# Performance work log

Measured on AMD Instinct MI355X. Metric: run time of the kernel, lower is better.

## Reference

```python
import jax, jax.numpy as jnp
import numpy as np

N, E, D, H, C, G = 20000, 160000, 128, 4, 3, 512
IN_F, EF = 74, 11


def setup_inputs():
    key = jax.random.key(0)
    ks = jax.random.split(key, 20)
    rn = lambda k, shape, s=0.05: jax.random.normal(k, shape, jnp.float32) * s
    return {
        "h0": rn(ks[0], (N, IN_F), 1.0),
        "e_f": rn(ks[1], (E, EF), 1.0),
        "src": jax.random.randint(ks[2], (E,), 0, N, jnp.int32),
        "dst": jax.random.randint(ks[3], (E,), 0, N, jnp.int32),
        "node_gid": jnp.sort(jax.random.randint(ks[4], (N,), 0, G, jnp.int32)),
        "num_graphs": G,
        "lin0_W": rn(ks[5], (H, IN_F, D)),
        "lin_W": rn(ks[6], (C - 1, H, D, D)),
        "We_W": rn(ks[7], (C, H, EF, D)),
        "Wq_W": rn(ks[8], (C, H, D, D)),
        "Wk_W": rn(ks[9], (C, H, D, D)),
        "Wv_W": rn(ks[10], (C, H, D, D)),
        "ln_g": jnp.ones((C, H, D), jnp.float32),
        "ln_b": jnp.zeros((C, H, D), jnp.float32),
        "out_W": rn(ks[11], (C, H * D, D)),
        "out_b": jnp.zeros((C, D), jnp.float32),
        "proj_W": rn(ks[12], (IN_F, D)),
        "proj_b": jnp.zeros((D,), jnp.float32),
        "gru_Wih0": rn(ks[13], (2, D, 3 * D)),
        "gru_Whh0": rn(ks[14], (2, D, 3 * D)),
        "gru_bih0": jnp.zeros((2, 3 * D), jnp.float32),
        "gru_bhh0": jnp.zeros((2, 3 * D), jnp.float32),
        "gru_Wih1": rn(ks[15], (2, 2 * D, 3 * D)),
        "gru_Whh1": rn(ks[16], (2, D, 3 * D)),
        "gru_bih1": jnp.zeros((2, 3 * D), jnp.float32),
        "gru_bhh1": jnp.zeros((2, 3 * D), jnp.float32),
    }


def _seg_mean(x, ids, n):
    s = jax.ops.segment_sum(x, ids, num_segments=n)
    c = jax.ops.segment_sum(jnp.ones((x.shape[0], 1), x.dtype), ids, num_segments=n)
    return s / jnp.maximum(c, 1.0)


def _layernorm(x, g, b, eps=1e-5):
    m = jnp.mean(x, -1, keepdims=True)
    v = jnp.var(x, -1, keepdims=True)
    return (x - m) * jax.lax.rsqrt(v + eps) * g + b


def _gat_head(h, ef_raw, src, dst, n, Wl, We, Wq, Wk, Wv, g, b):
    z = h @ Wl                                  # [N, D]
    ef = ef_raw @ We                            # [E, D]
    x = jnp.stack([z[src], z[dst], ef], axis=1)  # [E, 3, D]
    Q = jnp.einsum('eid,df->eif', x, Wq)
    K = jnp.einsum('eid,df->eif', x, Wk)
    V = jnp.einsum('eid,df->eif', x, Wv)
    attn = jax.nn.softmax(jnp.einsum('eid,ejd->eij', Q, K), axis=-1)  # [E,3,3]
    m = jnp.einsum('eij,ejd->ed', attn, V)      # (attn @ V).sum(1)
    h_new = _seg_mean(m, dst, n)                # mean over incoming edges
    return _layernorm(jax.nn.relu(h_new), g, b)


def _gru_dir(xs, Wih, Whh, bih, bhh, reverse):
    # xs: [T, B, in]; torch gate order r, z, n
    def step(h, x):
        gi = x @ Wih + bih
        gh = h @ Whh + bhh
        ir, iz, inn = jnp.split(gi, 3, axis=-1)
        hr, hz, hn = jnp.split(gh, 3, axis=-1)
        r = jax.nn.sigmoid(ir + hr)
        zg = jax.nn.sigmoid(iz + hz)
        ng = jnp.tanh(inn + r * hn)
        h_new = (1.0 - zg) * ng + zg * h
        return h_new, h_new
    h0 = jnp.zeros((xs.shape[1], Whh.shape[0]), xs.dtype)
    hT, ys = jax.lax.scan(step, h0, xs, reverse=reverse)
    return hT, ys


def _forward(h0, e_f, lin0_W, lin_W, We_W, Wq_W, Wk_W, Wv_W, ln_g, ln_b,
             out_W, out_b, proj_W, proj_b,
             gru_Wih0, gru_Whh0, gru_bih0, gru_bhh0,
             gru_Wih1, gru_Whh1, gru_bih1, gru_bhh1,
             src, dst, node_gid, num_graphs):
    n = h0.shape[0]
    conv_nums, head_nums = We_W.shape[0], We_W.shape[1]
    gru_list = [_seg_mean(h0, node_gid, num_graphs)]
    h = h0
    for j in range(conv_nums):
        heads = [_gat_head(h, e_f, src, dst, n,
                           lin0_W[i] if j == 0 else lin_W[j - 1, i],
                           We_W[j, i], Wq_W[j, i], Wk_W[j, i], Wv_W[j, i],
                           ln_g[j, i], ln_b[j, i])
                 for i in range(head_nums)]
        h = jnp.concatenate(heads, axis=1) @ out_W[j] + out_b[j]
        gru_list.append(_seg_mean(h, node_gid, num_graphs))
    # GRU readout: project initial 74-dim readout, seq = [proj, h1..hC]
    x0 = gru_list[0] @ proj_W + proj_b
    seq = jnp.stack([x0] + gru_list[1:], axis=0)  # [T, G, D]
    hf0, yf0 = _gru_dir(seq, gru_Wih0[0], gru_Whh0[0], gru_bih0[0], gru_bhh0[0], False)
    hb0, yb0 = _gru_dir(seq, gru_Wih0[1], gru_Whh0[1], gru_bih0[1], gru_bhh0[1], True)
    seq1 = jnp.concatenate([yf0, yb0], axis=-1)   # [T, G, 2D]
    hf1, _ = _gru_dir(seq1, gru_Wih1[0], gru_Whh1[0], gru_bih1[0], gru_bhh1[0], False)
    hb1, _ = _gru_dir(seq1, gru_Wih1[1], gru_Whh1[1], gru_bih1[1], gru_bhh1[1], True)
    # torch returns sum over the [num_layers*2, G, D] final hidden stack
    return hf0 + hb0 + hf1 + hb1


def reference(h0, e_f, src, dst, node_gid, num_graphs, lin0_W, lin_W, We_W,
              Wq_W, Wk_W, Wv_W, ln_g, ln_b, out_W, out_b, proj_W, proj_b,
              gru_Wih0, gru_Whh0, gru_bih0, gru_bhh0,
              gru_Wih1, gru_Whh1, gru_bih1, gru_bhh1):
    return _forward(h0, e_f, lin0_W, lin_W, We_W, Wq_W, Wk_W, Wv_W, ln_g, ln_b,
                    out_W, out_b, proj_W, proj_b,
                    gru_Wih0, gru_Whh0, gru_bih0, gru_bhh0,
                    gru_Wih1, gru_Whh1, gru_bih1, gru_bhh1,
                    src, dst, node_gid, num_graphs)
```

## Files before the change

kernel.cpp:

```cpp
#include <hip/hip_runtime.h>
#include <cstdint>

#define D_   128
#define H_   4
#define C_   3
#define G_   512
#define INF_ 74
#define EF_  11
#define T_   4
#define NW_  48

typedef __attribute__((ext_vector_type(8))) short bf16x8;
typedef __attribute__((ext_vector_type(4))) float f32x4;

__device__ inline unsigned short f2bf(float x) {
  unsigned u = __float_as_uint(x);
  unsigned r = u + 0x7fffu + ((u >> 16) & 1u);
  return (unsigned short)(r >> 16);
}
__device__ inline float bf2f(unsigned short x) {
  return __uint_as_float(((unsigned)x) << 16);
}
__device__ inline void unpack8(uint4 u, float* f) {
  f[0] = __uint_as_float(u.x << 16); f[1] = __uint_as_float(u.x & 0xffff0000u);
  f[2] = __uint_as_float(u.y << 16); f[3] = __uint_as_float(u.y & 0xffff0000u);
  f[4] = __uint_as_float(u.z << 16); f[5] = __uint_as_float(u.z & 0xffff0000u);
  f[6] = __uint_as_float(u.w << 16); f[7] = __uint_as_float(u.w & 0xffff0000u);
}

struct WDesc { const float* src; unsigned short* dst; int K; int D; int trans; };
struct WPack { WDesc d[NW_]; };

__global__ __launch_bounds__(256) void k_wcvt(WPack wp)
{
  WDesc w = wp.d[blockIdx.y];
  int tot = w.K * w.D;
  for (int i = blockIdx.x * 256 + threadIdx.x; i < tot; i += gridDim.x * 256) {
    if (w.trans) {
      int d = i / w.K, k = i - d * w.K;
      w.dst[i] = f2bf(w.src[(size_t)k * w.D + d]);
    } else {
      w.dst[i] = f2bf(w.src[i]);
    }
  }
}

__global__ __launch_bounds__(128) void k_small1(
    const float* __restrict__ WeW, const float* __restrict__ WqW,
    const float* __restrict__ WkW, const float* __restrict__ WvW,
    float* __restrict__ WeQ, float* __restrict__ WeK, float* __restrict__ WeV,
    float* __restrict__ GqT, float* __restrict__ GcT)
{
  int ch = blockIdx.x, f = blockIdx.y;
  const float* We = WeW + (size_t)ch * EF_ * 128 + f * 128;
  const float* Wq = WqW + (size_t)ch * 16384;
  const float* Wk = WkW + (size_t)ch * 16384;
  const float* Wv = WvW + (size_t)ch * 16384;
  __shared__ float sWe[128], sQ[128], sK[128];
  int d = threadIdx.x;
  sWe[d] = We[d];
  __syncthreads();
  float aq = 0.f, ak = 0.f, av = 0.f;
  for (int k = 0; k < 128; k++) {
    float w = sWe[k];
    aq += w * Wq[k * 128 + d];
    ak += w * Wk[k * 128 + d];
    av += w * Wv[k * 128 + d];
  }
  size_t off = (size_t)ch * EF_ * 128 + f * 128 + d;
  WeQ[off] = aq; WeK[off] = ak; WeV[off] = av;
  sQ[d] = aq; sK[d] = ak;
  __syncthreads();
  float gq = 0.f, gc = 0.f;
  for (int k = 0; k < 128; k++) {
    gq += Wq[(size_t)d * 128 + k] * sK[k];
    gc += Wk[(size_t)d * 128 + k] * sQ[k];
  }
  GqT[off] = gq; GcT[off] = gc;
}

__global__ __launch_bounds__(128) void k_small2(
    const float* __restrict__ WeQ, const float* __restrict__ WeK,
    float* __restrict__ M2)
{
  int ch = blockIdx.x;
  __shared__ float sQ[EF_ * 128], sK[EF_ * 128];
  int t = threadIdx.x;
  for (int i = t; i < EF_ * 128; i += 128) {
    sQ[i] = WeQ[(size_t)ch * EF_ * 128 + i];
    sK[i] = WeK[(size_t)ch * EF_ * 128 + i];
  }
  __syncthreads();
  if (t < EF_ * EF_) {
    int a = t / EF_, b = t % EF_;
    float s = 0.f;
    for (int k = 0; k < 128; k++) s += sQ[a * 128 + k] * sK[b * 128 + k];
    M2[(size_t)ch * (EF_ * EF_) + t] = s;
  }
}

__global__ __launch_bounds__(256) void k_utbt(
    const float* __restrict__ Mbuf, unsigned short* __restrict__ UTBt)
{
  int ch = blockIdx.x, slot = blockIdx.y;
  unsigned short* dst = UTBt + (size_t)ch * 32768 + slot * 16384;
  for (int i = threadIdx.x; i < 16384; i += 256) {
    int r = i >> 7, k = i & 127;
    float v = (slot == 0) ? Mbuf[(size_t)ch * 16384 + i]
                          : Mbuf[(size_t)ch * 16384 + k * 128 + r];
    dst[i] = f2bf(v);
  }
}

__global__ __launch_bounds__(128) void k_bcfold(
    const float* __restrict__ lin0, const float* __restrict__ linW,
    const float* __restrict__ GqT, const float* __restrict__ GcT,
    unsigned short* __restrict__ Wbc)
{
  int j = blockIdx.x, col = blockIdx.y;
  int K = (j == 0) ? INF_ : 128;
  int h = col >> 5, c2 = col & 31;
  __shared__ float sG[128];
  int t = threadIdx.x;
  if (c2 < 2 * EF_) {
    int f = (c2 < EF_) ? c2 : c2 - EF_;
    const float* G = ((c2 < EF_) ? GqT : GcT) +
                     ((size_t)(j * H_ + h) * EF_ + f) * 128;
    sG[t] = G[t];
  }
  __syncthreads();
  if (t < K) {
    float v = 0.f;
    if (c2 < 2 * EF_) {
      const float* lin = (j == 0)
          ? lin0 + (size_t)h * INF_ * 128 + t * 128
          : linW + ((size_t)(j - 1) * H_ + h) * 16384 + t * 128;
      for (int d = 0; d < 128; d++) v += lin[d] * sG[d];
    }
    Wbc[(size_t)j * 16384 + col * K + t] = f2bf(v);
  }
}

template <typename AT>
__global__ __launch_bounds__(256) void k_mfma(
    const AT* __restrict__ A, int lda, int aOffZ, int M, int K,
    const unsigned short* __restrict__ Bt, int btOffY, int btOffZ,
    float* __restrict__ outF, int ldc, int cOffY, int cOffZ,
    const float* __restrict__ bias,
    unsigned short* __restrict__ outH, int hStride, int hOffY, int hOffZ)
{
  const int bx = blockIdx.x, by = blockIdx.y, bz = blockIdx.z;
  A += (size_t)bz * aOffZ;
  const unsigned short* Bp = Bt + (size_t)by * btOffY + (size_t)bz * btOffZ;
  const int rowBase = bx * 128;
  __shared__ unsigned short As[128][40];
  __shared__ unsigned short Bs[128][40];
  const int t = threadIdx.x;
  const int w = t >> 6, l = t & 63;
  const int wr = w >> 1, wc = w & 1;
  const int fr = l & 15, fq = l >> 4;
  f32x4 acc[4][4];
#pragma unroll
  for (int m = 0; m < 4; m++)
#pragma unroll
    for (int n = 0; n < 4; n++) acc[m][n] = (f32x4){0.f, 0.f, 0.f, 0.f};

  const int sr = t >> 1, sh = t & 1;
  const int arow = rowBase + sr;
  const AT* aBase = A + (size_t)arow * lda;

  for (int k0 = 0; k0 < K; k0 += 32) {
    int kb = k0 + sh * 16;
    if constexpr (sizeof(AT) == 4) {
      unsigned short tmp[16];
      if (arow < M && kb + 16 <= K) {
        const AT* ap = aBase + kb;
#pragma unroll
        for (int i = 0; i < 16; i++) tmp[i] = f2bf(ap[i]);
      } else {
#pragma unroll
        for (int i = 0; i < 16; i++) {
          int gk = kb + i;
          float v = (arow < M && gk < K) ? (float)aBase[gk] : 0.f;
          tmp[i] = f2bf(v);
        }
      }
      *(uint4*)&As[sr][sh * 16]     = *(const uint4*)&tmp[0];
      *(uint4*)&As[sr][sh * 16 + 8] = *(const uint4*)&tmp[8];
    } else {
      if (arow < M && kb + 16 <= K) {
        const unsigned short* ap = (const unsigned short*)aBase + kb;
        *(uint4*)&As[sr][sh * 16]     = *(const uint4*)(ap);
        *(uint4*)&As[sr][sh * 16 + 8] = *(const uint4*)(ap + 8);
      } else {
#pragma unroll
        for (int i = 0; i < 16; i++) {
          int gk = kb + i;
          As[sr][sh * 16 + i] = (arow < M && gk < K)
              ? ((const unsigned short*)aBase)[gk] : (unsigned short)0;
        }
      }
    }
    if (t < 128) {
      unsigned short tmp[32];
      if (k0 + 32 <= K) {
        const unsigned short* bp = Bp + (size_t)t * K + k0;
#pragma unroll
        for (int i = 0; i < 32; i++) tmp[i] = bp[i];
      } else {
#pragma unroll
        for (int i = 0; i < 32; i++) {
          int gk = k0 + i;
          tmp[i] = (gk < K) ? Bp[(size_t)t * K + gk] : (unsigned short)0;
        }
      }
#pragma unroll
      for (int i = 0; i < 4; i++) *(uint4*)&Bs[t][i * 8] = *(const uint4*)&tmp[i * 8];
    }
    __syncthreads();
    bf16x8 af[4], bfr[4];
#pragma unroll
    for (int m = 0; m < 4; m++) af[m]  = *(const bf16x8*)&As[wr * 64 + m * 16 + fr][fq * 8];
#pragma unroll
    for (int n = 0; n < 4; n++) bfr[n] = *(const bf16x8*)&Bs[wc * 64 + n * 16 + fr][fq * 8];
#pragma unroll
    for (int m = 0; m < 4; m++)
#pragma unroll
      for (int n = 0; n < 4; n++)
        acc[m][n] = __builtin_amdgcn_mfma_f32_16x16x32_bf16(af[m], bfr[n], acc[m][n], 0, 0, 0);
    __syncthreads();
  }
#pragma unroll
  for (int m = 0; m < 4; m++) {
    int row0 = rowBase + wr * 64 + m * 16 + fq * 4;
#pragma unroll
    for (int n = 0; n < 4; n++) {
      int col = wc * 64 + n * 16 + fr;
#pragma unroll
      for (int r = 0; r < 4; r++) {
        int row = row0 + r;
        if (row < M) {
          float v = acc[m][n][r];
          if (outH) {
            outH[(size_t)row * hStride + by * hOffY + bz * hOffZ + col] = f2bf(v);
          } else {
            if (bias) v += bias[col];
            outF[(size_t)row * ldc + by * cOffY + bz * cOffZ + col] = v;
          }
        }
      }
    }
  }
}

__global__ void k_hist(const int* __restrict__ dst, int* __restrict__ deg, int E)
{
  int e = blockIdx.x * blockDim.x + threadIdx.x;
  if (e < E) atomicAdd(&deg[dst[e]], 1);
}

__global__ __launch_bounds__(1024) void k_scan(const int* __restrict__ deg,
                                               int* __restrict__ rowp, int N)
{
  __shared__ int part[1024];
  int t = threadIdx.x;
  int chunk = (N + 1023) / 1024;
  int base = t * chunk;
  int s = 0;
  for (int i = 0; i < chunk; i++) { int idx = base + i; if (idx < N) s += deg[idx]; }
  part[t] = s;
  __syncthreads();
  for (int off = 1; off < 1024; off <<= 1) {
    int v = (t >= off) ? part[t - off] : 0;
    __syncthreads();
    part[t] += v;
    __syncthreads();
  }
  int run = part[t] - s;
  for (int i = 0; i < chunk; i++) {
    int idx = base + i;
    if (idx < N) { rowp[idx] = run; run += deg[idx]; }
  }
  if (t == 1023) rowp[N] = part[1023];
}

__global__ void k_fill(const int* __restrict__ src, const int* __restrict__ dst,
                       const int* __restrict__ rowp, int* __restrict__ cursor,
                       int* __restrict__ eids, int* __restrict__ src_perm,
                       int* __restrict__ dst_perm, int E)
{
  int e = blockIdx.x * blockDim.x + threadIdx.x;
  if (e < E) {
    int d = dst[e];
    int pos = atomicAdd(&cursor[d], 1);
    int slot = rowp[d] + pos;
    eids[slot] = e;
    src_perm[slot] = src[e];
    dst_perm[slot] = d;
  }
}

__global__ void k_efperm(const float* __restrict__ e_f, const int* __restrict__ eids,
                         float* __restrict__ ef_perm, int E)
{
  int i = blockIdx.x * blockDim.x + threadIdx.x;
  if (i < E * EF_) {
    int idx = i / EF_, f = i - idx * EF_;
    ef_perm[i] = e_f[(size_t)eids[idx] * EF_ + f];
  }
}

__global__ __launch_bounds__(128) void k_wve(
    const float* __restrict__ WvW, const float* __restrict__ WeV,
    unsigned short* __restrict__ WvE)
{
  int ch = blockIdx.x;
  const float* Wv  = WvW + (size_t)ch * 16384;
  const float* wev = WeV + (size_t)ch * EF_ * 128;
  unsigned short* dst = WvE + (size_t)ch * 20480;
  for (int i = threadIdx.x; i < 20480; i += 128) {
    int d = i / 160, k = i - d * 160;
    float v = (k < 128) ? Wv[(size_t)k * 128 + d]
            : (k < 128 + EF_) ? wev[(size_t)(k - 128) * 128 + d] : 0.f;
    dst[i] = f2bf(v);
  }
}

__global__ __launch_bounds__(256) void k_ss(
    const unsigned short* __restrict__ Zb, const unsigned short* __restrict__ UTb,
    float* __restrict__ ss, int N)
{
  int h = threadIdx.x >> 6, lane = threadIdx.x & 63;
  int n = blockIdx.x;
  unsigned uz = *(const unsigned*)(Zb + (size_t)n * 512 + h * 128 + 2 * lane);
  unsigned uu = *(const unsigned*)(UTb + (size_t)n * 1024 + h * 256 + 2 * lane);
  float zx = __uint_as_float(uz << 16), zy = __uint_as_float(uz & 0xffff0000u);
  float ux = __uint_as_float(uu << 16), uy = __uint_as_float(uu & 0xffff0000u);
  float p = zx * ux + zy * uy;
#pragma unroll
  for (int m = 32; m; m >>= 1) p += __shfl_xor(p, m, 64);
  if (lane == 0) ss[n * H_ + h] = p;
}

__global__ __launch_bounds__(256) void k_elog(
    const unsigned short* __restrict__ BCb, const float* __restrict__ ss,
    const float* __restrict__ M2, const float* __restrict__ ef_perm,
    const int* __restrict__ src_perm, const int* __restrict__ dst_perm,
    float* __restrict__ elog, int E, int layer)
{
  int i0 = blockIdx.x * 64;
  __shared__ float efs[64 * EF_];
  __shared__ float m2s[4 * EF_ * EF_];
  int t = threadIdx.x;
  for (int i = t; i < 64 * EF_; i += 256) {
    int gi = i0 * EF_ + i;
    efs[i] = (gi < E * EF_) ? ef_perm[gi] : 0.f;
  }
  for (int i = t; i < 4 * EF_ * EF_; i += 256)
    m2s[i] = M2[(size_t)layer * 4 * EF_ * EF_ + i];
  __syncthreads();
  int sl = t >> 2, h = t & 3;
  int idx = i0 + sl;
  if (idx < E) {
    int s = src_perm[idx], d = dst_perm[idx];
    const float* ef = &efs[sl * EF_];
    const float* m2 = &m2s[h * EF_ * EF_];
    float ee = 0.f;
#pragma unroll
    for (int a = 0; a < EF_; a++) {
      float r = 0.f;
#pragma unroll
      for (int b = 0; b < EF_; b++) r += m2[a * EF_ + b] * ef[b];
      ee += ef[a] * r;
    }
    const unsigned short* bs = BCb + (size_t)s * 128 + h * 32;
    const unsigned short* bd = BCb + (size_t)d * 128 + h * 32;
    float se = 0.f, es = 0.f, de = 0.f, ed = 0.f;
#pragma unroll
    for (int f = 0; f < EF_; f++) {
      float e = ef[f];
      se += bf2f(bs[f]) * e;
      es += bf2f(bs[EF_ + f]) * e;
      de += bf2f(bd[f]) * e;
      ed += bf2f(bd[EF_ + f]) * e;
    }
    float* o = elog + ((size_t)idx * H_ + h) * 6;
    o[0] = ss[s * H_ + h];
    o[1] = se; o[2] = de; o[3] = es; o[4] = ed; o[5] = ee;
  }
}

__global__ __launch_bounds__(256) void k_edge(
    const unsigned short* __restrict__ Zb, const unsigned short* __restrict__ UTb,
    const float* __restrict__ ss, const float* __restrict__ elog,
    const float* __restrict__ ef_perm, const int* __restrict__ rowp,
    const int* __restrict__ src_perm, unsigned short* __restrict__ aggZE, int N)
{
  const int w = threadIdx.x >> 6;
  const int lane = threadIdx.x & 63;
  const int h = lane >> 4;
  const int q = lane & 15;
  const int lb = lane & 48;
  const int n = blockIdx.x;

  float zd[8], ud[8], td[8];
  unpack8(*(const uint4*)(Zb + (size_t)n * 512 + lane * 8), zd);
  const unsigned short* utp = UTb + (size_t)n * 1024 + h * 256 + q * 8;
  unpack8(*(const uint4*)(utp), ud);
  unpack8(*(const uint4*)(utp + 128), td);
  const float essd = __expf(ss[n * H_ + h]);
  const int beg = rowp[n], end = rowp[n + 1];
  float acc[8];
#pragma unroll
  for (int i = 0; i < 8; i++) acc[i] = 0.f;
  float wdsum = 0.f, a11 = 0.f;

  for (int idx = beg + w; idx < end; idx += 4) {
    int s = src_perm[idx];
    float zs[8];
    unpack8(*(const uint4*)(Zb + (size_t)s * 512 + lane * 8), zs);
    float v1 = 0.f, v2 = 0.f;
#pragma unroll
    for (int i = 0; i < 8; i++) {
      v1 += zs[i] * ud[i];
      v2 += zs[i] * td[i];
    }
#pragma unroll
    for (int m = 1; m < 16; m <<= 1) {
      v1 += __shfl_xor(v1, m, 64);
      v2 += __shfl_xor(v2, m, 64);
    }
    float lv = (q < 6) ? elog[((size_t)idx * H_ + h) * 6 + q] : 0.f;
    float S00 = __shfl(lv, lb + 0, 64);
    float S02 = __shfl(lv, lb + 1, 64);
    float S12 = __shfl(lv, lb + 2, 64);
    float S20 = __shfl(lv, lb + 3, 64);
    float S21 = __shfl(lv, lb + 4, 64);
    float S22 = __shfl(lv, lb + 5, 64);
    float e00 = __expf(S00), e01 = __expf(v1), e02 = __expf(S02);
    float i0r = 1.f / (e00 + e01 + e02);
    float e10 = __expf(v2), e12 = __expf(S12);
    float i1r = 1.f / (e10 + essd + e12);
    float e20 = __expf(S20), e21 = __expf(S21), e22 = __expf(S22);
    float i2r = 1.f / (e20 + e21 + e22);
    float w0 = e00 * i0r + e10 * i1r + e20 * i2r;
    float w1 = e01 * i0r + essd * i1r + e21 * i2r;
    float w2 = e02 * i0r + e12 * i1r + e22 * i2r;
#pragma unroll
    for (int i = 0; i < 8; i++) acc[i] += w0 * zs[i];
    wdsum += w1;
    float efl = (q < EF_) ? ef_perm[(size_t)idx * EF_ + q] : 0.f;
    a11 += w2 * efl;
  }
  __shared__ float red[4][64][10];
#pragma unroll
  for (int i = 0; i < 8; i++) red[w][lane][i] = acc[i];
  red[w][lane][8] = wdsum;
  red[w][lane][9] = a11;
  __syncthreads();
  if (w == 0) {
    float a[8], wd = 0.f, a1 = 0.f;
#pragma unroll
    for (int i = 0; i < 8; i++)
      a[i] = red[0][lane][i] + red[1][lane][i] + red[2][lane][i] + red[3][lane][i];
    wd = red[0][lane][8] + red[1][lane][8] + red[2][lane][8] + red[3][lane][8];
    a1 = red[0][lane][9] + red[1][lane][9] + red[2][lane][9] + red[3][lane][9];
    int cnt = end - beg;
    float invc = (cnt > 0) ? 1.f / (float)cnt : 1.f;
    unsigned short* ob = aggZE + (size_t)n * 640 + h * 160;
    unsigned short tmp[8];
#pragma unroll
    for (int i = 0; i < 8; i++) tmp[i] = f2bf((a[i] + wd * zd[i]) * invc);
    *(uint4*)(ob + q * 8) = *(const uint4*)&tmp[0];
    ob[128 + q] = (q < EF_) ? f2bf(a1 * invc) : (unsigned short)0;
    ob[144 + q] = 0;
  }
}

__global__ __launch_bounds__(256) void k_ln(
    float* __restrict__ zh, const float* __restrict__ lng,
    const float* __restrict__ lnb, int N, int layer)
{
  int h = threadIdx.x >> 6, lane = threadIdx.x & 63;
  int n = blockIdx.x;
  float* p = zh + (size_t)n * 512 + h * 128 + 2 * lane;
  float2 v = *(const float2*)p;
  v.x = fmaxf(v.x, 0.f); v.y = fmaxf(v.y, 0.f);
  float s1 = v.x + v.y;
#pragma unroll
  for (int m = 32; m; m >>= 1) s1 += __shfl_xor(s1, m, 64);
  float mean = s1 * (1.f / 128.f);
  float dx = v.x - mean, dy = v.y - mean;
  float s2 = dx * dx + dy * dy;
#pragma unroll
  for (int m = 32; m; m >>= 1) s2 += __shfl_xor(s2, m, 64);
  float rstd = rsqrtf(s2 * (1.f / 128.f) + 1e-5f);
  int gi = (layer * H_ + h) * 128 + 2 * lane;
  float2 g2 = *(const float2*)&lng[gi];
  float2 b2 = *(const float2*)&lnb[gi];
  float2 o;
  o.x = dx * rstd * g2.x + b2.x;
  o.y = dy * rstd * g2.y + b2.y;
  *(float2*)p = o;
}

__global__ void k_gmean(const float* __restrict__ X, const int* __restrict__ gid,
                        float* __restrict__ outp, int N, int ld)
{
  int g = blockIdx.x, part = blockIdx.y;
  int lo = 0, hi = N;
  while (lo < hi) { int m = (lo + hi) >> 1; if (gid[m] < g) lo = m + 1; else hi = m; }
  int s0 = lo;
  lo = s0; hi = N;
  while (lo < hi) { int m = (lo + hi) >> 1; if (gid[m] < g + 1) lo = m + 1; else hi = m; }
  int s1 = lo;
  int cnt = s1 - s0;
  float inv = 1.f / (float)(cnt > 0 ? cnt : 1);
  int r0 = s0 + (cnt * part) / 4;
  int r1 = s0 + (cnt * (part + 1)) / 4;
  if (r1 <= r0) return;
  for (int d = threadIdx.x; d < ld; d += blockDim.x) {
    float s = 0.f;
    for (int n = r0; n < r1; n++) s += X[(size_t)n * ld + d];
    atomicAdd(&outp[(size_t)g * ld + d], s * inv);
  }
}

__global__ __launch_bounds__(384) void k_gruR(
    const float* __restrict__ gi, const float* __restrict__ Whh,
    const float* __restrict__ bih, const float* __restrict__ bhh,
    float* __restrict__ yout, float* __restrict__ hfinal)
{
  const int g = blockIdx.x, dir = blockIdx.y, t = threadIdx.x;
  const float* W = Whh + (size_t)dir * 128 * 384 + t;
  const float bi = bih[dir * 384 + t];
  const float bh = bhh[dir * 384 + t];
  __shared__ float hb[128];
  __shared__ float rb[128], zb[128], nb[128];
  if (t < 128) hb[t] = 0.f;
  __syncthreads();
  for (int st = 0; st < T_; st++) {
    int ts = dir ? (T_ - 1 - st) : st;
    float acc = bh;
    for (int k = 0; k < 128; k++) acc += hb[k] * W[(size_t)k * 384];
    float gv = gi[((size_t)ts * G_ + g) * 768 + dir * 384 + t] + bi;
    if (t < 128) {
      rb[t] = 1.f / (1.f + __expf(-(gv + acc)));
    } else if (t < 256) {
      zb[t - 128] = 1.f / (1.f + __expf(-(gv + acc)));
    }
    __syncthreads();
    if (t >= 256) nb[t - 256] = tanhf(gv + rb[t - 256] * acc);
    __syncthreads();
    if (t < 128) {
      float z = zb[t];
      float h = (1.f - z) * nb[t] + z * hb[t];
      hb[t] = h;
      if (yout) yout[((size_t)ts * G_ + g) * 256 + dir * 128 + t] = h;
    }
    __syncthreads();
  }
  if (t < 128) hfinal[((size_t)dir * G_ + g) * 128 + t] = hb[t];
}

__global__ void k_final(const float* __restrict__ fp, float* __restrict__ outp, int n)
{
  int i = blockIdx.x * blockDim.x + threadIdx.x;
  if (i < n) {
    outp[i] = fp[i] + fp[G_ * 128 + i] + fp[2 * G_ * 128 + i] + fp[3 * G_ * 128 + i];
  }
}

extern "C" void kernel_launch(void* const* d_in, const int* in_sizes, int n_in,
                              void* d_out, int out_size, void* d_ws, size_t ws_size,
                              hipStream_t stream)
{
  (void)n_in; (void)ws_size;
  const float* h0   = (const float*)d_in[0];
  const float* e_f  = (const float*)d_in[1];
  const int*   srcI = (const int*)d_in[2];
  const int*   dstI = (const int*)d_in[3];
  const int*   gid  = (const int*)d_in[4];
  const float* lin0 = (const float*)d_in[6];
  const float* linW = (const float*)d_in[7];
  const float* WeW  = (const float*)d_in[8];
  const float* WqW  = (const float*)d_in[9];
  const float* WkW  = (const float*)d_in[10];
  const float* WvW  = (const float*)d_in[11];
  const float* lng  = (const float*)d_in[12];
  const float* lnb  = (const float*)d_in[13];
  const float* outW = (const float*)d_in[14];
  const float* outb = (const float*)d_in[15];
  const float* projW= (const float*)d_in[16];
  const float* projb= (const float*)d_in[17];
  const float* Wih0 = (const float*)d_in[18];
  const float* Whh0 = (const float*)d_in[19];
  const float* bih0 = (const float*)d_in[20];
  const float* bhh0 = (const float*)d_in[21];
  const float* Wih1 = (const float*)d_in[22];
  const float* Whh1 = (const float*)d_in[23];
  const float* bih1 = (const float*)d_in[24];
  const float* bhh1 = (const float*)d_in[25];
  float* outp = (float*)d_out;

  const int N = in_sizes[0] / INF_;
  const int E = in_sizes[2];

  char* wp = (char*)d_ws;
  auto alloc = [&](size_t bytes) -> void* {
    void* p = (void*)wp;
    wp += (bytes + 255) & ~(size_t)255;
    return p;
  };
  unsigned short* Zb  = (unsigned short*)alloc((size_t)N * 512 * 2);
  unsigned short* UTb = (unsigned short*)alloc((size_t)N * 1024 * 2);
  unsigned short* BCb = (unsigned short*)alloc((size_t)N * 128 * 2);
  unsigned short* aggZE = (unsigned short*)alloc((size_t)N * 640 * 2);
  float* zh   = (float*)alloc((size_t)N * 512 * 4);
  float* hcur = (float*)alloc((size_t)N * 128 * 4);
  float* ssb  = (float*)alloc((size_t)N * H_ * 4);
  float* elog = (float*)alloc((size_t)E * H_ * 6 * 4);
  float* efp  = (float*)alloc((size_t)E * EF_ * 4);
  float* WeQ  = (float*)alloc((size_t)C_ * H_ * EF_ * 128 * 4);
  float* WeK  = (float*)alloc((size_t)C_ * H_ * EF_ * 128 * 4);
  float* WeV  = (float*)alloc((size_t)C_ * H_ * EF_ * 128 * 4);
  float* M2   = (float*)alloc((size_t)C_ * H_ * EF_ * EF_ * 4);
  float* GqT  = (float*)alloc((size_t)C_ * H_ * EF_ * 128 * 4);
  float* GcT  = (float*)alloc((size_t)C_ * H_ * EF_ * 128 * 4);
  float* Mbuf = (float*)alloc((size_t)C_ * H_ * 16384 * 4);
  unsigned short* WkPl  = (unsigned short*)alloc((size_t)C_ * H_ * 16384 * 2);
  unsigned short* UTBt  = (unsigned short*)alloc((size_t)C_ * H_ * 2 * 16384 * 2);
  unsigned short* WbcBt = (unsigned short*)alloc((size_t)C_ * 16384 * 2);
  unsigned short* WvE   = (unsigned short*)alloc((size_t)C_ * H_ * 20480 * 2);
  unsigned short* linBt0 = (unsigned short*)alloc((size_t)4 * 128 * INF_ * 2);
  unsigned short* linBt12= (unsigned short*)alloc((size_t)2 * 512 * 128 * 2);
  unsigned short* outBt  = (unsigned short*)alloc((size_t)C_ * 128 * 512 * 2);
  unsigned short* projBt = (unsigned short*)alloc((size_t)128 * INF_ * 2);
  unsigned short* WihBt0 = (unsigned short*)alloc((size_t)768 * 128 * 2);
  unsigned short* WihBt1 = (unsigned short*)alloc((size_t)768 * 256 * 2);
  float* gibuf = (float*)alloc((size_t)T_ * G_ * 768 * 4);
  int* deg    = (int*)alloc((size_t)N * 4);
  int* cursor = (int*)alloc((size_t)N * 4);
  int* rowp   = (int*)alloc((size_t)(N + 1) * 4);
  int* eids   = (int*)alloc((size_t)E * 4);
  int* srcp   = (int*)alloc((size_t)E * 4);
  int* dstp   = (int*)alloc((size_t)E * 4);
  float* gm74 = (float*)alloc((size_t)G_ * INF_ * 4);
  float* seq  = (float*)alloc((size_t)T_ * G_ * 128 * 4);
  float* seq1 = (float*)alloc((size_t)T_ * G_ * 256 * 4);
  float* fparts=(float*)alloc((size_t)4 * G_ * 128 * 4);

  const int gM = (N + 127) / 128;

  hipMemsetAsync(deg, 0, (size_t)N * 4, stream);
  hipMemsetAsync(cursor, 0, (size_t)N * 4, stream);
  hipMemsetAsync(gm74, 0, (size_t)G_ * INF_ * 4, stream);
  hipMemsetAsync(seq, 0, (size_t)T_ * G_ * 128 * 4, stream);
  k_hist<<<(E + 255) / 256, 256, 0, stream>>>(dstI, deg, E);
  k_scan<<<1, 1024, 0, stream>>>(deg, rowp, N);
  k_fill<<<(E + 255) / 256, 256, 0, stream>>>(srcI, dstI, rowp, cursor,
                                              eids, srcp, dstp, E);
  k_efperm<<<(E * EF_ + 255) / 256, 256, 0, stream>>>(e_f, eids, efp, E);

  k_small1<<<dim3(C_ * H_, EF_), 128, 0, stream>>>(WeW, WqW, WkW, WvW,
                                                   WeQ, WeK, WeV, GqT, GcT);
  k_small2<<<C_ * H_, 128, 0, stream>>>(WeQ, WeK, M2);
  k_wve<<<C_ * H_, 128, 0, stream>>>(WvW, WeV, WvE);
  k_bcfold<<<dim3(C_, 128), 128, 0, stream>>>(lin0, linW, GqT, GcT, WbcBt);

  {
    WPack w{};
    int nw = 0;
    auto addw = [&](const float* s, unsigned short* d, int K, int D, int tr) {
      w.d[nw].src = s; w.d[nw].dst = d; w.d[nw].K = K; w.d[nw].D = D;
      w.d[nw].trans = tr; nw++;
    };
    for (int h = 0; h < 4; h++)
      addw(lin0 + (size_t)h * INF_ * 128, linBt0 + (size_t)h * 128 * INF_, INF_, 128, 1);
    for (int j = 1; j < 3; j++)
      for (int h = 0; h < 4; h++)
        addw(linW + ((size_t)(j - 1) * 4 + h) * 16384,
             linBt12 + (size_t)(j - 1) * 65536 + (size_t)h * 16384, 128, 128, 1);
    for (int j = 0; j < 3; j++)
      addw(outW + (size_t)j * 65536, outBt + (size_t)j * 65536, 512, 128, 1);
    addw(projW, projBt, INF_, 128, 1);
    for (int ch = 0; ch < 12; ch++)
      addw(WkW + (size_t)ch * 16384, WkPl + (size_t)ch * 16384, 128, 128, 0);
    for (int dir = 0; dir < 2; dir++) {
      addw(Wih0 + (size_t)dir * 128 * 384, WihBt0 + (size_t)dir * 384 * 128,
           128, 384, 1);
      addw(Wih1 + (size_t)dir * 256 * 384, WihBt1 + (size_t)dir * 384 * 256,
           256, 384, 1);
    }
    k_wcvt<<<dim3(64, nw), 256, 0, stream>>>(w);
  }

  k_mfma<float><<<dim3(1, 1, 12), 256, 0, stream>>>(
      WqW, 128, 16384, 128, 128, WkPl, 0, 16384,
      Mbuf, 128, 0, 16384, nullptr, nullptr, 0, 0, 0);

  k_utbt<<<dim3(12, 2), 256, 0, stream>>>(Mbuf, UTBt);

  k_gmean<<<dim3(G_, 4), 128, 0, stream>>>(h0, gid, gm74, N, INF_);
  k_mfma<float><<<dim3(4, 1, 1), 256, 0, stream>>>(
      gm74, INF_, 0, G_, INF_, projBt, 0, 0,
      seq, 128, 0, 0, projb, nullptr, 0, 0, 0);

  for (int j = 0; j < C_; j++) {
    const float* Ain = (j == 0) ? h0 : hcur;
    const int Kin = (j == 0) ? INF_ : 128;
    if (j == 0)
      k_mfma<float><<<dim3(gM, 4, 1), 256, 0, stream>>>(
          h0, INF_, 0, N, INF_, linBt0, 128 * INF_, 0,
          nullptr, 0, 0, 0, nullptr, Zb, 512, 128, 0);
    else
      k_mfma<float><<<dim3(gM, 4, 1), 256, 0, stream>>>(
          hcur, 128, 0, N, 128, linBt12 + (size_t)(j - 1) * 65536, 16384, 0,
          nullptr, 0, 0, 0, nullptr, Zb, 512, 128, 0);
    k_mfma<float><<<dim3(gM, 1, 1), 256, 0, stream>>>(
        Ain, Kin, 0, N, Kin, WbcBt + (size_t)j * 16384, 0, 0,
        nullptr, 0, 0, 0, nullptr, BCb, 128, 0, 0);
    k_mfma<unsigned short><<<dim3(gM, 2, 4), 256, 0, stream>>>(
        Zb, 512, 128, N, 128, UTBt + (size_t)j * 4 * 32768, 16384, 32768,
        nullptr, 0, 0, 0, nullptr, UTb, 1024, 128, 256);
    k_ss<<<N, 256, 0, stream>>>(Zb, UTb, ssb, N);
    k_elog<<<(E + 63) / 64, 256, 0, stream>>>(BCb, ssb, M2, efp, srcp, dstp,
                                              elog, E, j);
    k_edge<<<N, 256, 0, stream>>>(Zb, UTb, ssb, elog, efp, rowp, srcp, aggZE, N);
    k_mfma<unsigned short><<<dim3(gM, 1, 4), 256, 0, stream>>>(
        aggZE, 640, 160, N, 160, WvE + (size_t)j * 4 * 20480, 0, 20480,
        zh, 512, 0, 128, nullptr, nullptr, 0, 0, 0);
    k_ln<<<N, 256, 0, stream>>>(zh, lng, lnb, N, j);
    k_mfma<float><<<dim3(gM, 1, 1), 256, 0, stream>>>(
        zh, 512, 0, N, 512, outBt + (size_t)j * 65536, 0, 0,
        hcur, 128, 0, 0, outb + j * 128, nullptr, 0, 0, 0);
    k_gmean<<<dim3(G_, 4), 128, 0, stream>>>(hcur, gid,
                                             seq + (size_t)(j + 1) * G_ * 128, N, 128);
  }

  k_mfma<float><<<dim3(16, 6, 1), 256, 0, stream>>>(
      seq, 128, 0, T_ * G_, 128, WihBt0, 128 * 128, 0,
      gibuf, 768, 128, 0, nullptr, nullptr, 0, 0, 0);
  k_gruR<<<dim3(G_, 2), 384, 0, stream>>>(gibuf, Whh0, bih0, bhh0,
                                          seq1, fparts);
  k_mfma<float><<<dim3(16, 6, 1), 256, 0, stream>>>(
      seq1, 256, 0, T_ * G_, 256, WihBt1, 128 * 256, 0,
      gibuf, 768, 128, 0, nullptr, nullptr, 0, 0, 0);
  k_gruR<<<dim3(G_, 2), 384, 0, stream>>>(gibuf, Whh1, bih1, bhh1,
                                          nullptr, fparts + 2 * G_ * 128);
  k_final<<<(out_size + 255) / 256, 256, 0, stream>>>(fparts, outp, out_size);
}
```

Measured before the change: 1.168 ms.

## Fuse value GEMM with ReLU+LayerNorm, store bf16, swizzle blocks across XCDs

Replaces the per-head value GEMM and separate ReLU+LayerNorm kernel with one fused MFMA kernel. It computes row statistics in registers via cross-lane shuffles and shared memory, then writes normalized output as bf16. This removes an fp32 write and re-read of the N×512 intermediate and one launch, and halves the input bytes of the following output GEMM. It also remaps block indices in the edge kernels to group consecutive work per XCD for L2 locality. Computing variance as E[x²]−mean² in one pass, plus bf16 storage, slightly reduces numerical accuracy.

```diff
diff --git a/kernel.cpp b/kernel.cpp
--- a/kernel.cpp
+++ b/kernel.cpp
@@ -26,6 +26,12 @@
   f[2] = __uint_as_float(u.y << 16); f[3] = __uint_as_float(u.y & 0xffff0000u);
   f[4] = __uint_as_float(u.z << 16); f[5] = __uint_as_float(u.z & 0xffff0000u);
   f[6] = __uint_as_float(u.w << 16); f[7] = __uint_as_float(u.w & 0xffff0000u);
+}
+__device__ inline int xcd_swz(int bid, int nwg) {
+  int q = nwg >> 3, r = nwg & 7;
+  int xcd = bid & 7, off = bid >> 3;
+  int base = (xcd < r) ? xcd * (q + 1) : r * (q + 1) + (xcd - r) * q;
+  return base + off;
 }
 
 struct WDesc { const float* src; unsigned short* dst; int K; int D; int trans; };
@@ -253,6 +259,116 @@
   }
 }
 
+__global__ __launch_bounds__(256) void k_mfmaLN(
+    const unsigned short* __restrict__ A, int M,
+    const unsigned short* __restrict__ Bt,
+    const float* __restrict__ lng, const float* __restrict__ lnb, int layer,
+    unsigned short* __restrict__ zh)
+{
+  const int bx = blockIdx.x, h = blockIdx.y;
+  const int K = 160;
+  A += (size_t)h * 160;
+  const unsigned short* Bp = Bt + (size_t)h * 20480;
+  const int rowBase = bx * 128;
+  __shared__ unsigned short As[128][40];
+  __shared__ unsigned short Bs[128][40];
+  __shared__ float rsum[128][2][2];
+  const int t = threadIdx.x;
+  const int w = t >> 6, l = t & 63;
+  const int wr = w >> 1, wc = w & 1;
+  const int fr = l & 15, fq = l >> 4;
+  f32x4 acc[4][4];
+#pragma unroll
+  for (int m = 0; m < 4; m++)
+#pragma unroll
+    for (int n = 0; n < 4; n++) acc[m][n] = (f32x4){0.f, 0.f, 0.f, 0.f};
+
+  const int sr = t >> 1, sh = t & 1;
+  const int arow = rowBase + sr;
+  const unsigned short* aBase = A + (size_t)arow * 640;
+
+  for (int k0 = 0; k0 < K; k0 += 32) {
+    int kb = k0 + sh * 16;
+    if (arow < M) {
+      *(uint4*)&As[sr][sh * 16]     = *(const uint4*)(aBase + kb);
+      *(uint4*)&As[sr][sh * 16 + 8] = *(const uint4*)(aBase + kb + 8);
+    } else {
+#pragma unroll
+      for (int i = 0; i < 16; i++) As[sr][sh * 16 + i] = 0;
+    }
+    if (t < 128) {
+      const unsigned short* bp = Bp + (size_t)t * K + k0;
+#pragma unroll
+      for (int i = 0; i < 4; i++) *(uint4*)&Bs[t][i * 8] = *(const uint4*)(bp + i * 8);
+    }
+    __syncthreads();
+    bf16x8 af[4], bfr[4];
+#pragma unroll
+    for (int m = 0; m < 4; m++) af[m]  = *(const bf16x8*)&As[wr * 64 + m * 16 + fr][fq * 8];
+#pragma unroll
+    for (int n = 0; n < 4; n++) bfr[n] = *(const bf16x8*)&Bs[wc * 64 + n * 16 + fr][fq * 8];
+#pragma unroll
+    for (int m = 0; m < 4; m++)
+#pragma unroll
+      for (int n = 0; n < 4; n++)
+        acc[m][n] = __builtin_amdgcn_mfma_f32_16x16x32_bf16(af[m], bfr[n], acc[m][n], 0, 0, 0);
+    __syncthreads();
+  }
+#pragma unroll
+  for (int m = 0; m < 4; m++)
+#pragma unroll
+    for (int n = 0; n < 4; n++)
+#pragma unroll
+      for (int r = 0; r < 4; r++)
+        acc[m][n][r] = fmaxf(acc[m][n][r], 0.f);
+#pragma unroll
+  for (int m = 0; m < 4; m++) {
+#pragma unroll
+    for (int r = 0; r < 4; r++) {
+      float s1 = 0.f, s2 = 0.f;
+#pragma unroll
+      for (int n = 0; n < 4; n++) {
+        float v = acc[m][n][r];
+        s1 += v; s2 += v * v;
+      }
+#pragma unroll
+      for (int msk = 1; msk < 16; msk <<= 1) {
+        s1 += __shfl_xor(s1, msk, 64);
+        s2 += __shfl_xor(s2, msk, 64);
+      }
+      if (fr == 0) {
+        int lr = wr * 64 + m * 16 + fq * 4 + r;
+        rsum[lr][wc][0] = s1;
+        rsum[lr][wc][1] = s2;
+      }
+    }
+  }
+  __syncthreads();
+#pragma unroll
+  for (int n = 0; n < 4; n++) {
+    int col = wc * 64 + n * 16 + fr;
+    int gci = (layer * H_ + h) * 128 + col;
+    float g = lng[gci], b = lnb[gci];
+#pragma unroll
+    for (int m = 0; m < 4; m++) {
+#pragma unroll
+      for (int r = 0; r < 4; r++) {
+        int lr = wr * 64 + m * 16 + fq * 4 + r;
+        int row = rowBase + lr;
+        if (row < M) {
+          float s1 = rsum[lr][0][0] + rsum[lr][1][0];
+          float s2 = rsum[lr][0][1] + rsum[lr][1][1];
+          float mean = s1 * (1.f / 128.f);
+          float var = s2 * (1.f / 128.f) - mean * mean;
+          float rstd = rsqrtf(var + 1e-5f);
+          float v = (acc[m][n][r] - mean) * rstd * g + b;
+          zh[(size_t)row * 512 + h * 128 + col] = f2bf(v);
+        }
+      }
+    }
+  }
+}
+
 __global__ void k_hist(const int* __restrict__ dst, int* __restrict__ deg, int E)
 {
   int e = blockIdx.x * blockDim.x + threadIdx.x;
@@ -348,7 +464,7 @@
     const int* __restrict__ src_perm, const int* __restrict__ dst_perm,
     float* __restrict__ elog, int E, int layer)
 {
-  int i0 = blockIdx.x * 64;
+  int i0 = xcd_swz(blockIdx.x, gridDim.x) * 64;
   __shared__ float efs[64 * EF_];
   __shared__ float m2s[4 * EF_ * EF_];
   int t = threadIdx.x;
@@ -401,7 +517,7 @@
   const int h = lane >> 4;
   const int q = lane & 15;
   const int lb = lane & 48;
-  const int n = blockIdx.x;
+  const int n = xcd_swz(blockIdx.x, N);
 
   float zd[8], ud[8], td[8];
   unpack8(*(const uint4*)(Zb + (size_t)n * 512 + lane * 8), zd);
@@ -475,33 +591,6 @@
     ob[128 + q] = (q < EF_) ? f2bf(a1 * invc) : (unsigned short)0;
     ob[144 + q] = 0;
   }
-}
-
-__global__ __launch_bounds__(256) void k_ln(
-    float* __restrict__ zh, const float* __restrict__ lng,
-    const float* __restrict__ lnb, int N, int layer)
-{
-  int h = threadIdx.x >> 6, lane = threadIdx.x & 63;
-  int n = blockIdx.x;
-  float* p = zh + (size_t)n * 512 + h * 128 + 2 * lane;
-  float2 v = *(const float2*)p;
-  v.x = fmaxf(v.x, 0.f); v.y = fmaxf(v.y, 0.f);
-  float s1 = v.x + v.y;
-#pragma unroll
-  for (int m = 32; m; m >>= 1) s1 += __shfl_xor(s1, m, 64);
-  float mean = s1 * (1.f / 128.f);
-  float dx = v.x - mean, dy = v.y - mean;
-  float s2 = dx * dx + dy * dy;
-#pragma unroll
-  for (int m = 32; m; m >>= 1) s2 += __shfl_xor(s2, m, 64);
-  float rstd = rsqrtf(s2 * (1.f / 128.f) + 1e-5f);
-  int gi = (layer * H_ + h) * 128 + 2 * lane;
-  float2 g2 = *(const float2*)&lng[gi];
-  float2 b2 = *(const float2*)&lnb[gi];
-  float2 o;
-  o.x = dx * rstd * g2.x + b2.x;
-  o.y = dy * rstd * g2.y + b2.y;
-  *(float2*)p = o;
 }
 
 __global__ void k_gmean(const float* __restrict__ X, const int* __restrict__ gid,
@@ -616,7 +705,7 @@
   unsigned short* UTb = (unsigned short*)alloc((size_t)N * 1024 * 2);
   unsigned short* BCb = (unsigned short*)alloc((size_t)N * 128 * 2);
   unsigned short* aggZE = (unsigned short*)alloc((size_t)N * 640 * 2);
-  float* zh   = (float*)alloc((size_t)N * 512 * 4);
+  unsigned short* zh  = (unsigned short*)alloc((size_t)N * 512 * 2);
   float* hcur = (float*)alloc((size_t)N * 128 * 4);
   float* ssb  = (float*)alloc((size_t)N * H_ * 4);
   float* elog = (float*)alloc((size_t)E * H_ * 6 * 4);
@@ -727,11 +816,9 @@
     k_elog<<<(E + 63) / 64, 256, 0, stream>>>(BCb, ssb, M2, efp, srcp, dstp,
                                               elog, E, j);
     k_edge<<<N, 256, 0, stream>>>(Zb, UTb, ssb, elog, efp, rowp, srcp, aggZE, N);
-    k_mfma<unsigned short><<<dim3(gM, 1, 4), 256, 0, stream>>>(
-        aggZE, 640, 160, N, 160, WvE + (size_t)j * 4 * 20480, 0, 20480,
-        zh, 512, 0, 128, nullptr, nullptr, 0, 0, 0);
-    k_ln<<<N, 256, 0, stream>>>(zh, lng, lnb, N, j);
-    k_mfma<float><<<dim3(gM, 1, 1), 256, 0, stream>>>(
+    k_mfmaLN<<<dim3(gM, H_), 256, 0, stream>>>(
+        aggZE, N, WvE + (size_t)j * 4 * 20480, lng, lnb, j, zh);
+    k_mfma<unsigned short><<<dim3(gM, 1, 1), 256, 0, stream>>>(
         zh, 512, 0, N, 512, outBt + (size_t)j * 65536, 0, 0,
         hcur, 128, 0, 0, outb + j * 128, nullptr, 0, 0, 0);
     k_gmean<<<dim3(G_, 4), 128, 0, stream>>>(hcur, gid,
```

Result: no change. 1.150 ms (-1.6%).
